# Kernel tuning notes

Measured on AMD Instinct MI355X. Metric: run time of the kernel, lower is better.

Reference implementation:

```python
import jax, jax.numpy as jnp
import numpy as np

# ---- static config (mirrors module init / config constants) ----
STATE_DIM = 512
D_H = 2048
INPUT_DIM = 1024
N_QUBITS = 6
N_VQC_LAYERS = 3
MSD = 128                 # mamba_state_dim (last dim of padded state)
PAD_SLICES = 16           # padded slice count in h_padded
MIN_T = 1e-6              # control_limits.min_value
REL_STEP = 0.1            # control_limits.hardware_relative_step
ABS_STEP = 1e-4           # control_limits.hardware_absolute_step
MAX_T = 0.05              # control_limits.max_value
DIM = 2 ** N_QUBITS

# qubit 0 = most significant bit (matches reshape-based gate application)
_BITS = ((np.arange(DIM)[:, None] >> np.arange(N_QUBITS)[None, ::-1]) & 1).astype(np.float32)
_sign = np.ones(DIM, np.float32)
for k in range(N_QUBITS):  # ring CZ entanglement
    k2 = (k + 1) % N_QUBITS
    _sign *= 1.0 - 2.0 * _BITS[:, k] * _BITS[:, k2]
CZ_SIGN = jnp.asarray(_sign)
Z_OBS = jnp.asarray((1.0 - 2.0 * _BITS).mean(axis=1))  # mean <Z_k> observable weights


def _apply_ry(state, ang, k):
    # state: [B, 2^n] real statevector; ang: [B] rotation angle on qubit k
    B = state.shape[0]
    s = state.reshape(B, 2 ** k, 2, 2 ** (N_QUBITS - k - 1))
    c = jnp.cos(ang / 2)[:, None, None]
    si = jnp.sin(ang / 2)[:, None, None]
    a0, a1 = s[:, :, 0, :], s[:, :, 1, :]
    out = jnp.stack([c * a0 - si * a1, si * a0 + c * a1], axis=2)
    return out.reshape(B, DIM)


def _vqc(feats, enc_W, enc_b, thetas):
    # EvolutionTimeVQCLayer: angle-encode features, layered RY + ring CZ, mean-Z expectation
    B = feats.shape[0]
    angles = feats @ enc_W + enc_b  # [B, n_qubits]
    state = jnp.zeros((B, DIM), feats.dtype).at[:, 0].set(1.0)
    for k in range(N_QUBITS):
        state = _apply_ry(state, angles[:, k], k)
    for l in range(N_VQC_LAYERS):
        for k in range(N_QUBITS):
            state = _apply_ry(state, jnp.broadcast_to(thetas[l, k], (B,)), k)
        state = state * CZ_SIGN[None, :]
    return (state * state) @ Z_OBS  # [B]


def _hamiltonian(q, p, x, W1, b1, W2, b2, W3, b3):
    z = jnp.concatenate([q, p, x], axis=-1)          # [B, 2*S + D]
    h1 = jnp.tanh(z @ W1 + b1)
    h2 = jnp.tanh(h1 @ W2 + b2)
    return (h2 @ W3)[:, 0] + b3                       # [B] scalar energy per sample


def setup_inputs() -> dict:
    key = jax.random.key(0)
    ks = jax.random.split(key, 12)
    def glorot(k, shape):
        std = np.sqrt(2.0 / (shape[0] + shape[-1]))
        return jax.random.normal(k, shape, jnp.float32) * std
    B = 2048
    h_in = 2 * STATE_DIM + INPUT_DIM
    gen_in = INPUT_DIM + 2 * STATE_DIM
    return {
        'x': jax.random.normal(ks[0], (B, INPUT_DIM), jnp.float32),
        'h_padded': jax.random.normal(ks[1], (B, PAD_SLICES, MSD), jnp.float32),
        'aux_padded': jnp.zeros((B, PAD_SLICES, MSD), jnp.float32),
        'W1': glorot(ks[2], (h_in, D_H)), 'b1': jnp.zeros((D_H,), jnp.float32),
        'W2': glorot(ks[3], (D_H, D_H)), 'b2': jnp.zeros((D_H,), jnp.float32),
        'W3': glorot(ks[4], (D_H, 1)), 'b3': jnp.zeros((), jnp.float32),
        'W_out': glorot(ks[5], (2 * STATE_DIM, INPUT_DIM)),
        'b_out': jnp.zeros((INPUT_DIM,), jnp.float32),
        'enc_W': glorot(ks[6], (gen_in, N_QUBITS)) * 0.1,
        'enc_b': jnp.zeros((N_QUBITS,), jnp.float32),
        'thetas': jax.random.normal(ks[7], (N_VQC_LAYERS, N_QUBITS), jnp.float32) * 0.1,
        'gain': jnp.asarray(0.1, jnp.float32),
        'shift': jnp.asarray(7.0, jnp.float32),
        'cap_param': jnp.asarray(0.02, jnp.float32),
        'time_bias': jnp.asarray(0.0005, jnp.float32),
        'last_stable': jnp.asarray(0.0005, jnp.float32),
    }


def reference(x, h_padded, aux_padded, W1, b1, W2, b2, W3, b3, W_out, b_out,
              enc_W, enc_b, thetas, gain, shift, cap_param, time_bias, last_stable):
    B = x.shape[0]
    total = 2 * STATE_DIM
    num_slices = total // MSD
    # unpack phase-space state from padded mamba-shaped state
    unpacked = h_padded[:, :num_slices, :].reshape(B, total)
    q_t, p_t = jnp.split(unpacked, 2, axis=-1)

    # ---- evolution-time generation via VQC ----
    ctrl = jnp.concatenate([x, q_t, p_t], axis=-1)
    samples = _vqc(ctrl, enc_W, enc_b, thetas)                       # [B]
    soft_gain = jax.nn.softplus(gain)
    soft_shift = jax.nn.softplus(shift)
    adjusted = jax.nn.softplus(soft_gain * samples - soft_shift)
    raw = jnp.mean(adjusted) + time_bias
    cap = jnp.maximum(jax.nn.softplus(cap_param), 1e-6)
    evo = cap * jax.nn.sigmoid(raw / cap)
    evo = jnp.where(jnp.isfinite(evo), evo, cap * jax.nn.sigmoid(time_bias / cap))
    prev = jnp.maximum(last_stable, MIN_T)
    cand = jnp.maximum(evo, MIN_T)
    max_step = jnp.maximum(prev * REL_STEP, ABS_STEP)
    cand = jnp.minimum(cand, prev + max_step)
    cand = jnp.minimum(cand, MAX_T)
    dt = jnp.where(jnp.isfinite(cand), cand, prev)                   # scalar

    # ---- fused HNN symplectic (leapfrog) step ----
    def H_sum(q, p):
        return _hamiltonian(q, p, x, W1, b1, W2, b2, W3, b3).sum()
    grad_qp = jax.grad(H_sum, argnums=(0, 1))
    dHdq0, _ = grad_qp(q_t, p_t)
    p_half = p_t - 0.5 * dt * dHdq0
    _, dHdp_h = grad_qp(q_t, p_half)
    q_next = q_t + dt * dHdp_h
    dHdq_n, _ = grad_qp(q_next, p_half)
    p_next = p_half - 0.5 * dt * dHdq_n

    out = jnp.concatenate([q_next, p_next], axis=-1) @ W_out + b_out  # [B, INPUT_DIM]

    # repack state into padded mamba layout
    new_slices = jnp.concatenate([q_next, p_next], axis=-1).reshape(B, num_slices, MSD)
    pad = jnp.zeros((B, PAD_SLICES - num_slices, MSD), out.dtype)
    h_next = jnp.concatenate([new_slices, pad], axis=1)
    return out, h_next
```

## Files before the change

kernel.cpp:

```cpp
#include <hip/hip_runtime.h>
#include <math.h>

#define NB 2048
#define ZD 2048
#define SD 512
#define NELEM_Z (NB * ZD)
#define MB_ (1024 * 1024)

typedef float f32x4 __attribute__((ext_vector_type(4)));
typedef __bf16 bf16x8 __attribute__((ext_vector_type(8)));
typedef __bf16 bf16x4 __attribute__((ext_vector_type(4)));

__device__ __forceinline__ float softplus_f(float x) {
  if (x > 20.f) return x;
  if (x < -20.f) return expf(x);
  return log1pf(expf(x));
}

__device__ __forceinline__ void gload_lds16(const __bf16* g, __bf16* l) {
  __builtin_amdgcn_global_load_lds(
      (__attribute__((address_space(1))) void*)(g),
      (__attribute__((address_space(3))) void*)(l), 16, 0, 0);
}

__device__ __forceinline__ int pack_fp8x4(float a, float b, float c, float d) {
  int p = __builtin_amdgcn_cvt_pk_fp8_f32(a, b, 0, false);
  p = __builtin_amdgcn_cvt_pk_fp8_f32(c, d, p, true);
  return p;
}
__device__ __forceinline__ float fp8_to_f32(unsigned char b) {
  return __builtin_amdgcn_cvt_f32_fp8((int)b, 0);
}

__global__ void build_z_kernel(const float* __restrict__ x,
                               const float* __restrict__ h_padded,
                               float* __restrict__ z,
                               __bf16* __restrict__ zb,
                               unsigned char* __restrict__ zf8,
                               float* __restrict__ acc) {
  int t = blockIdx.x * blockDim.x + threadIdx.x;
  if (t == 0) acc[0] = 0.f;
  int b = t >> 9;
  int i4 = t & 511;
  f32x4 v = (i4 < 256) ? ((const f32x4*)h_padded)[t]
                       : ((const f32x4*)x)[b * 256 + (i4 - 256)];
  ((f32x4*)z)[t] = v;
  bf16x4 o;
  o[0] = (__bf16)v[0]; o[1] = (__bf16)v[1];
  o[2] = (__bf16)v[2]; o[3] = (__bf16)v[3];
  ((bf16x4*)zb)[t] = o;
  ((int*)zf8)[t] = pack_fp8x4(v[0], v[1], v[2], v[3]);
}

__global__ void prep_w(const float* __restrict__ in,
                       __bf16* __restrict__ outT, int R, int C) {
  __shared__ float tile[32][33];
  int bx = blockIdx.x * 32, by = blockIdx.y * 32;
  int tx = threadIdx.x, ty = threadIdx.y;
  for (int r = ty; r < 32; r += 8)
    tile[r][tx] = in[(size_t)(by + r) * C + bx + tx];
  __syncthreads();
  for (int r = ty; r < 32; r += 8)
    outT[(size_t)(bx + r) * R + by + tx] = (__bf16)tile[tx][r];
}

__global__ void prep_w8(const float* __restrict__ in,
                        unsigned char* __restrict__ outN,
                        unsigned char* __restrict__ outT, int R, int C) {
  __shared__ float tile[32][33];
  int bx = blockIdx.x * 32, by = blockIdx.y * 32;
  int tx = threadIdx.x, ty = threadIdx.y;
  for (int r = ty; r < 32; r += 8) {
    float v = in[(size_t)(by + r) * C + bx + tx] * 16.f;
    tile[r][tx] = v;
    int p = __builtin_amdgcn_cvt_pk_fp8_f32(v, v, 0, false);
    outN[(size_t)(by + r) * C + bx + tx] = (unsigned char)(p & 0xff);
  }
  __syncthreads();
  for (int r = ty; r < 32; r += 8) {
    float v = tile[tx][r];
    int p = __builtin_amdgcn_cvt_pk_fp8_f32(v, v, 0, false);
    outT[(size_t)(bx + r) * R + by + tx] = (unsigned char)(p & 0xff);
  }
}

__global__ __launch_bounds__(256) void angles_kernel(
    const float* __restrict__ z,
    const float* __restrict__ enc_W,
    const float* __restrict__ enc_b,
    float* __restrict__ angles) {
  int w = threadIdx.x >> 6, lane = threadIdx.x & 63;
  int row = blockIdx.x * 4 + w;
  const float* zrow = z + (size_t)row * ZD;
  float pa[6] = {0.f, 0.f, 0.f, 0.f, 0.f, 0.f};
#pragma unroll
  for (int t = 0; t < 32; t++) {
    int j = t * 64 + lane;
    float c = (j < 1024) ? zrow[1024 + j] : zrow[j - 1024];
    const float* wp = enc_W + j * 6;
#pragma unroll
    for (int k = 0; k < 6; k++) pa[k] += c * wp[k];
  }
#pragma unroll
  for (int k = 0; k < 6; k++)
    for (int off = 32; off > 0; off >>= 1) pa[k] += __shfl_down(pa[k], off, 64);
  if (lane == 0) {
#pragma unroll
    for (int k = 0; k < 6; k++) angles[row * 6 + k] = pa[k] + enc_b[k];
  }
}

__global__ __launch_bounds__(64) void sim_kernel(
    const float* __restrict__ angles,
    const float* __restrict__ thetas,
    const float* __restrict__ gain,
    const float* __restrict__ shift,
    float* __restrict__ acc) {
  int row = blockIdx.x * 64 + threadIdx.x;
  const float* a = angles + row * 6;

  float s[64];
#pragma unroll
  for (int i = 0; i < 64; i++) s[i] = 0.f;
  s[0] = 1.f;

#pragma unroll
  for (int k = 0; k < 6; k++) {
    float half = 0.5f * a[k];
    float c = cosf(half), si = sinf(half);
    int m = 1 << (5 - k);
#pragma unroll
    for (int i = 0; i < 64; i++) {
      if ((i & m) == 0) {
        float a0 = s[i], a1 = s[i | m];
        s[i] = c * a0 - si * a1;
        s[i | m] = si * a0 + c * a1;
      }
    }
  }
#pragma unroll
  for (int l = 0; l < 3; l++) {
#pragma unroll
    for (int k = 0; k < 6; k++) {
      float half = 0.5f * thetas[l * 6 + k];
      float c = cosf(half), si = sinf(half);
      int m = 1 << (5 - k);
#pragma unroll
      for (int i = 0; i < 64; i++) {
        if ((i & m) == 0) {
          float a0 = s[i], a1 = s[i | m];
          s[i] = c * a0 - si * a1;
          s[i | m] = si * a0 + c * a1;
        }
      }
    }
#pragma unroll
    for (int i = 0; i < 64; i++) {
      int rot = ((i << 1) | (i >> 5)) & 63;
      if (__popc(i & rot) & 1) s[i] = -s[i];
    }
  }

  float val = 0.f;
#pragma unroll
  for (int i = 0; i < 64; i++) {
    float zo = (6.f - 2.f * (float)__popc(i)) * (1.f / 6.f);
    val += s[i] * s[i] * zo;
  }
  float sg = softplus_f(gain[0]);
  float ss = softplus_f(shift[0]);
  float adj = softplus_f(sg * val - ss);
  for (int off = 32; off > 0; off >>= 1) adj += __shfl_down(adj, off, 64);
  if (threadIdx.x == 0) atomicAdd(acc, adj);
}

__global__ void dt_kernel(const float* __restrict__ acc,
                          const float* __restrict__ cap_param,
                          const float* __restrict__ time_bias,
                          const float* __restrict__ last_stable,
                          float* __restrict__ dt_out) {
  float raw = acc[0] * (1.f / (float)NB) + time_bias[0];
  float cap = fmaxf(softplus_f(cap_param[0]), 1e-6f);
  float evo = cap / (1.f + expf(-raw / cap));
  if (!isfinite(evo)) evo = cap / (1.f + expf(-time_bias[0] / cap));
  float prev = fmaxf(last_stable[0], 1e-6f);
  float cand = fmaxf(evo, 1e-6f);
  float max_step = fmaxf(prev * 0.1f, 1e-4f);
  cand = fminf(cand, prev + max_step);
  cand = fminf(cand, 0.05f);
  dt_out[0] = isfinite(cand) ? cand : prev;
}

template <int EPI>
__global__ __launch_bounds__(256, 2) void mfma_gemm8(
    const unsigned char* __restrict__ A, int lda,
    const unsigned char* __restrict__ Bt, int ldb,
    void* __restrict__ Cv, int ldc,
    const float* __restrict__ bias,
    const float* __restrict__ w3,
    const unsigned char* __restrict__ aux, int ldaux,
    int Kslice) {
  __shared__ __align__(16) unsigned char sA[2 * 128 * 64];
  __shared__ __align__(16) unsigned char sB[2 * 64 * 64];

  const int tid = threadIdx.x;
  const int lane = tid & 63;
  const int w = tid >> 6;
  const int wm = w & 1, wn = w >> 1;
  const int row0 = blockIdx.y * 128;
  const int col0 = blockIdx.x * 64;
  const int koff = blockIdx.z * Kslice;

  const int mA0 = tid >> 2, cpA0 = tid & 3;
  const int mA1 = (256 + tid) >> 2, cpA1 = tid & 3;
  const int mB0 = tid >> 2, cpB0 = tid & 3;
  const unsigned char* gA0 = A + (size_t)(row0 + mA0) * lda + koff + cpA0 * 16;
  const unsigned char* gA1 = A + (size_t)(row0 + mA1) * lda + koff + cpA1 * 16;
  const unsigned char* gB0 = Bt + (size_t)(col0 + mB0) * ldb + koff + cpB0 * 16;
  const int wA0a = mA0 * 64 + (((2 * cpA0) + mA0) & 7) * 8;
  const int wA0b = mA0 * 64 + (((2 * cpA0 + 1) + mA0) & 7) * 8;
  const int wA1a = mA1 * 64 + (((2 * cpA1) + mA1) & 7) * 8;
  const int wA1b = mA1 * 64 + (((2 * cpA1 + 1) + mA1) & 7) * 8;
  const int wB0a = mB0 * 64 + (((2 * cpB0) + mB0) & 7) * 8;
  const int wB0b = mB0 * 64 + (((2 * cpB0 + 1) + mB0) & 7) * 8;

  const int q = lane >> 4, r = lane & 15;
  int aoff[4][2], boff[2][2];
#pragma unroll
  for (int i = 0; i < 4; i++) {
    int ma = wm * 64 + i * 16 + r;
#pragma unroll
    for (int h = 0; h < 2; h++)
      aoff[i][h] = ma * 64 + (((h * 4 + q) + ma) & 7) * 8;
  }
#pragma unroll
  for (int j = 0; j < 2; j++) {
    int mb = wn * 32 + j * 16 + r;
#pragma unroll
    for (int h = 0; h < 2; h++)
      boff[j][h] = mb * 64 + (((h * 4 + q) + mb) & 7) * 8;
  }

  f32x4 acc[4][2] = {};

  f32x4 rA0 = *(const f32x4*)gA0;
  f32x4 rA1 = *(const f32x4*)gA1;
  f32x4 rB0 = *(const f32x4*)gB0;
  *(long long*)(sA + wA0a) = ((const long long*)&rA0)[0];
  *(long long*)(sA + wA0b) = ((const long long*)&rA0)[1];
  *(long long*)(sA + wA1a) = ((const long long*)&rA1)[0];
  *(long long*)(sA + wA1b) = ((const long long*)&rA1)[1];
  *(long long*)(sB + wB0a) = ((const long long*)&rB0)[0];
  *(long long*)(sB + wB0b) = ((const long long*)&rB0)[1];
  __syncthreads();

  int cur = 0;
  for (int k0 = 0; k0 < Kslice; k0 += 64) {
    const bool more = (k0 + 64 < Kslice);
    if (more) {
      rA0 = *(const f32x4*)(gA0 + k0 + 64);
      rA1 = *(const f32x4*)(gA1 + k0 + 64);
      rB0 = *(const f32x4*)(gB0 + k0 + 64);
    }

    const unsigned char* bA = sA + cur * (128 * 64);
    const unsigned char* bB = sB + cur * (64 * 64);
#pragma unroll
    for (int h = 0; h < 2; h++) {
      long long af[4], bf[2];
#pragma unroll
      for (int i = 0; i < 4; i++) af[i] = *(const long long*)(bA + aoff[i][h]);
#pragma unroll
      for (int j = 0; j < 2; j++) bf[j] = *(const long long*)(bB + boff[j][h]);
#pragma unroll
      for (int i = 0; i < 4; i++)
#pragma unroll
        for (int j = 0; j < 2; j++)
          acc[i][j] = __builtin_amdgcn_mfma_f32_16x16x32_fp8_fp8(
              af[i], bf[j], acc[i][j], 0, 0, 0);
    }

    if (more) {
      unsigned char* nA = sA + (cur ^ 1) * (128 * 64);
      unsigned char* nB = sB + (cur ^ 1) * (64 * 64);
      *(long long*)(nA + wA0a) = ((const long long*)&rA0)[0];
      *(long long*)(nA + wA0b) = ((const long long*)&rA0)[1];
      *(long long*)(nA + wA1a) = ((const long long*)&rA1)[0];
      *(long long*)(nA + wA1b) = ((const long long*)&rA1)[1];
      *(long long*)(nB + wB0a) = ((const long long*)&rB0)[0];
      *(long long*)(nB + wB0b) = ((const long long*)&rB0)[1];
    }
    __syncthreads();
    cur ^= 1;
  }

  float* Cf = (float*)Cv;
  unsigned char* C8 = (unsigned char*)Cv;
  float* Pz = Cf + (size_t)blockIdx.z * (size_t)gridDim.y * 128 * ldc;

#pragma unroll
  for (int i = 0; i < 4; i++) {
    int rowb = row0 + wm * 64 + i * 16 + q * 4;
#pragma unroll
    for (int j = 0; j < 2; j++) {
      int col = col0 + wn * 32 + j * 16 + r;
      if (EPI == 0) {
#pragma unroll
        for (int g = 0; g < 4; g++)
          Pz[(size_t)(rowb + g) * ldc + col] = acc[i][j][g];
      } else {
        float o[4];
#pragma unroll
        for (int g = 0; g < 4; g++) {
          float v = acc[i][j][g] * 0.0625f;
          if (EPI == 1) {
            o[g] = tanhf(v + bias[col]);
          } else if (EPI == 2) {
            float t = tanhf(v + bias[col]);
            o[g] = 32.f * (1.f - t * t) * w3[col];
          } else {
            float h = fp8_to_f32(aux[(size_t)(rowb + g) * ldaux + col]);
            o[g] = v * (1.f - h * h);
          }
        }
        int p = pack_fp8x4(o[0], o[1], o[2], o[3]);
#pragma unroll
        for (int g = 0; g < 4; g++)
          C8[(size_t)(rowb + g) * ldc + col] =
              (unsigned char)((p >> (8 * g)) & 0xff);
      }
    }
  }
}

__global__ __launch_bounds__(256, 2) void mfma_gemm_bf16(
    const __bf16* __restrict__ A, int lda,
    const __bf16* __restrict__ Bt, int ldb,
    float* __restrict__ P, int ldc,
    int Kslice) {
  __shared__ __bf16 sA[2][128 * 64];
  __shared__ __bf16 sB[2][64 * 64];

  const int tid = threadIdx.x;
  const int lane = tid & 63;
  const int w = tid >> 6;
  const int wm = w & 1, wn = w >> 1;
  const int row0 = blockIdx.y * 128;
  const int col0 = blockIdx.x * 64;
  const int koff = blockIdx.z * Kslice;

  const __bf16* gA[4]; int lofA[4];
  const __bf16* gB[2]; int lofB[2];
#pragma unroll
  for (int i = 0; i < 4; i++) {
    int c = i * 256 + tid;
    int m = c >> 3, cc = c & 7;
    int o = cc ^ (m & 7);
    gA[i] = A + (size_t)(row0 + m) * lda + koff + o * 8;
    lofA[i] = c * 8;
  }
#pragma unroll
  for (int i = 0; i < 2; i++) {
    int c = i * 256 + tid;
    int m = c >> 3, cc = c & 7;
    int o = cc ^ (m & 7);
    gB[i] = Bt + (size_t)(col0 + m) * ldb + koff + o * 8;
    lofB[i] = c * 8;
  }

  const int q = lane >> 4, r = lane & 15;
  int aoff[4][2], boff[2][2];
#pragma unroll
  for (int i = 0; i < 4; i++) {
    int ma = wm * 64 + i * 16 + r;
#pragma unroll
    for (int h = 0; h < 2; h++)
      aoff[i][h] = (ma * 8 + ((h * 4 + q) ^ (ma & 7))) * 8;
  }
#pragma unroll
  for (int j = 0; j < 2; j++) {
    int mb = wn * 32 + j * 16 + r;
#pragma unroll
    for (int h = 0; h < 2; h++)
      boff[j][h] = (mb * 8 + ((h * 4 + q) ^ (mb & 7))) * 8;
  }

  f32x4 acc[4][2] = {};

#pragma unroll
  for (int i = 0; i < 4; i++) gload_lds16(gA[i], &sA[0][0] + lofA[i]);
#pragma unroll
  for (int i = 0; i < 2; i++) gload_lds16(gB[i], &sB[0][0] + lofB[i]);

  int cur = 0;
  for (int k0 = 0; k0 < Kslice; k0 += 64) {
    __syncthreads();
    if (k0 + 64 < Kslice) {
      int nxt = cur ^ 1;
#pragma unroll
      for (int i = 0; i < 4; i++)
        gload_lds16(gA[i] + k0 + 64, &sA[nxt][0] + lofA[i]);
#pragma unroll
      for (int i = 0; i < 2; i++)
        gload_lds16(gB[i] + k0 + 64, &sB[nxt][0] + lofB[i]);
    }
#pragma unroll
    for (int h = 0; h < 2; h++) {
      bf16x8 af[4], bfr[2];
#pragma unroll
      for (int i = 0; i < 4; i++)
        af[i] = *(const bf16x8*)(&sA[cur][0] + aoff[i][h]);
#pragma unroll
      for (int j = 0; j < 2; j++)
        bfr[j] = *(const bf16x8*)(&sB[cur][0] + boff[j][h]);
#pragma unroll
      for (int i = 0; i < 4; i++)
#pragma unroll
        for (int j = 0; j < 2; j++)
          acc[i][j] = __builtin_amdgcn_mfma_f32_16x16x32_bf16(af[i], bfr[j],
                                                              acc[i][j], 0, 0, 0);
    }
    cur ^= 1;
  }

  float* Pz = P + (size_t)blockIdx.z * (size_t)gridDim.y * 128 * ldc;
#pragma unroll
  for (int i = 0; i < 4; i++) {
    int rowb = row0 + wm * 64 + i * 16 + q * 4;
#pragma unroll
    for (int j = 0; j < 2; j++) {
      int col = col0 + wn * 32 + j * 16 + r;
#pragma unroll
      for (int g = 0; g < 4; g++)
        Pz[(size_t)(rowb + g) * ldc + col] = acc[i][j][g];
    }
  }
}

__global__ void update_kernel(float* __restrict__ z, __bf16* __restrict__ zb,
                              unsigned char* __restrict__ zf8,
                              const float* __restrict__ gp,
                              const float* __restrict__ dt,
                              float coef, int off) {
  int t = blockIdx.x * blockDim.x + threadIdx.x;
  int b = t >> 7;
  int j4 = t & 127;
  const f32x4* g4 = (const f32x4*)gp;
  constexpr int STRIDE = NB * SD / 4;
  f32x4 g = g4[t] + g4[t + STRIDE] + g4[t + 2 * STRIDE] + g4[t + 3 * STRIDE];
  int zi4 = (b * ZD + off) / 4 + j4;
  f32x4 v = ((f32x4*)z)[zi4];
  float s = coef * dt[0] * (1.f / 512.f);
  v[0] += s * g[0]; v[1] += s * g[1]; v[2] += s * g[2]; v[3] += s * g[3];
  ((f32x4*)z)[zi4] = v;
  bf16x4 o;
  o[0] = (__bf16)v[0]; o[1] = (__bf16)v[1];
  o[2] = (__bf16)v[2]; o[3] = (__bf16)v[3];
  ((bf16x4*)zb)[zi4] = o;
  ((int*)zf8)[zi4] = pack_fp8x4(v[0], v[1], v[2], v[3]);
}

__global__ void wout_reduce(const float* __restrict__ gp,
                            const float* __restrict__ b_out,
                            float* __restrict__ out) {
  int t = blockIdx.x * blockDim.x + threadIdx.x;
  constexpr int S = NB * 1024 / 4;
  const f32x4* g4 = (const f32x4*)gp;
  f32x4 v = g4[t] + g4[t + S];
  f32x4 bb = ((const f32x4*)b_out)[t & 255];
  v[0] += bb[0]; v[1] += bb[1]; v[2] += bb[2]; v[3] += bb[3];
  ((f32x4*)out)[t] = v;
}

__global__ void hnext_kernel(const float* __restrict__ z,
                             float* __restrict__ out) {
  int t = blockIdx.x * blockDim.x + threadIdx.x;
  int i4 = t & 511;
  f32x4 zero = {0.f, 0.f, 0.f, 0.f};
  ((f32x4*)out)[t] = (i4 < 256) ? ((const f32x4*)z)[t] : zero;
}

extern "C" void kernel_launch(void* const* d_in, const int* in_sizes, int n_in,
                              void* d_out, int out_size, void* d_ws,
                              size_t ws_size, hipStream_t stream) {
  const float* x        = (const float*)d_in[0];
  const float* h_padded = (const float*)d_in[1];
  const float* W1    = (const float*)d_in[3];
  const float* b1    = (const float*)d_in[4];
  const float* W2    = (const float*)d_in[5];
  const float* b2    = (const float*)d_in[6];
  const float* W3    = (const float*)d_in[7];
  const float* W_out = (const float*)d_in[9];
  const float* b_out = (const float*)d_in[10];
  const float* enc_W = (const float*)d_in[11];
  const float* enc_b = (const float*)d_in[12];
  const float* thetas = (const float*)d_in[13];
  const float* gain   = (const float*)d_in[14];
  const float* shift  = (const float*)d_in[15];
  const float* cap_p  = (const float*)d_in[16];
  const float* t_bias = (const float*)d_in[17];
  const float* l_stab = (const float*)d_in[18];

  float* out_mat  = (float*)d_out;
  float* out_hnxt = (float*)d_out + NB * 1024;

  char* base = (char*)d_ws;
  float* z      = (float*)(base);
  float* part   = (float*)(base + 16 * MB_);
  __bf16* zb    = (__bf16*)(base + 32 * MB_);
  __bf16* Wot   = (__bf16*)(base + 40 * MB_);
  float* angl   = (float*)(base + 42 * MB_);
  float* accp   = (float*)(base + 42 * MB_ + 65536);
  float* dtp    = accp + 1;
  unsigned char* zf8  = (unsigned char*)(base + 43 * MB_);
  unsigned char* h1_8 = zf8 + (size_t)NELEM_Z;
  unsigned char* g2_8 = h1_8 + (size_t)NELEM_Z;
  unsigned char* g1_8 = g2_8 + (size_t)NELEM_Z;
  unsigned char* W1n8 = g1_8 + (size_t)NELEM_Z;
  unsigned char* W1t8 = W1n8 + (size_t)NELEM_Z;
  unsigned char* W2n8 = W1t8 + (size_t)NELEM_Z;
  unsigned char* W2t8 = W2n8 + (size_t)NELEM_Z;

  dim3 thr256(256);
  dim3 thrT(32, 8);

  prep_w8<<<dim3(64, 64), thrT, 0, stream>>>(W1, W1n8, W1t8, ZD, ZD);
  prep_w8<<<dim3(64, 64), thrT, 0, stream>>>(W2, W2n8, W2t8, ZD, ZD);
  prep_w<<<dim3(32, 32), thrT, 0, stream>>>(W_out, Wot, 1024, 1024);

  build_z_kernel<<<dim3(NELEM_Z / 4 / 256), thr256, 0, stream>>>(
      x, h_padded, z, zb, zf8, accp);
  angles_kernel<<<dim3(NB / 4), thr256, 0, stream>>>(z, enc_W, enc_b, angl);
  sim_kernel<<<dim3(NB / 64), dim3(64), 0, stream>>>(angl, thetas, gain, shift,
                                                     accp);
  dt_kernel<<<dim3(1), dim3(1), 0, stream>>>(accp, cap_p, t_bias, l_stab, dtp);

  const int   j0r[3]  = {0, 512, 0};
  const int   offs[3] = {512, 0, 512};
  const float coef[3] = {-0.5f, 1.0f, -0.5f};

  dim3 gridSq(32, 16, 1);
  dim3 gridGr(8, 16, 4);

  for (int i = 0; i < 3; i++) {
    mfma_gemm8<1><<<gridSq, thr256, 0, stream>>>(
        zf8, ZD, W1t8, ZD, h1_8, ZD, b1, nullptr, nullptr, 0, ZD);
    mfma_gemm8<2><<<gridSq, thr256, 0, stream>>>(
        h1_8, ZD, W2t8, ZD, g2_8, ZD, b2, W3, nullptr, 0, ZD);
    mfma_gemm8<3><<<gridSq, thr256, 0, stream>>>(
        g2_8, ZD, W2n8, ZD, g1_8, ZD, nullptr, nullptr, h1_8, ZD, ZD);
    mfma_gemm8<0><<<gridGr, thr256, 0, stream>>>(
        g1_8, ZD, W1n8 + (size_t)j0r[i] * ZD, ZD, part, SD, nullptr, nullptr,
        nullptr, 0, 512);
    update_kernel<<<dim3(NB * SD / 4 / 256), thr256, 0, stream>>>(
        z, zb, zf8, part, dtp, coef[i], offs[i]);
  }

  mfma_gemm_bf16<<<dim3(16, 16, 2), thr256, 0, stream>>>(zb, ZD, Wot, 1024,
                                                         part, 1024, 512);
  wout_reduce<<<dim3(NB * 1024 / 4 / 256), thr256, 0, stream>>>(part, b_out,
                                                                out_mat);

  hnext_kernel<<<dim3(NELEM_Z / 4 / 256), thr256, 0, stream>>>(z, out_hnxt);
}
```

Baseline: 481.4 us.

## Double GEMM K-tile to 128 with padded LDS and fuse angle encoding into z build

The FP8 MFMA GEMM now stages 128-wide K tiles in LDS with a 144-byte padded row stride instead of 64-wide XOR-swizzled tiles. Each fragment is fetched with one 16-byte LDS read that feeds two MFMAs, which halves the loop iterations and barriers. Separately, the VQC angle projection is folded into the z-building kernel, removing one launch and a reread of z. In exchange, LDS use per block roughly doubles and more prefetch registers are live, which may lower occupancy under the 2-blocks bound.

After: 445.9 us. -7.4%, faster.

```diff
diff --git a/kernel.cpp b/kernel.cpp
--- a/kernel.cpp
+++ b/kernel.cpp
@@ -10,6 +10,7 @@
 typedef float f32x4 __attribute__((ext_vector_type(4)));
 typedef __bf16 bf16x8 __attribute__((ext_vector_type(8)));
 typedef __bf16 bf16x4 __attribute__((ext_vector_type(4)));
+typedef long long i64;
 
 __device__ __forceinline__ float softplus_f(float x) {
   if (x > 20.f) return x;
@@ -32,24 +33,55 @@
   return __builtin_amdgcn_cvt_f32_fp8((int)b, 0);
 }
 
-__global__ void build_z_kernel(const float* __restrict__ x,
-                               const float* __restrict__ h_padded,
-                               float* __restrict__ z,
-                               __bf16* __restrict__ zb,
-                               unsigned char* __restrict__ zf8,
-                               float* __restrict__ acc) {
-  int t = blockIdx.x * blockDim.x + threadIdx.x;
-  if (t == 0) acc[0] = 0.f;
-  int b = t >> 9;
-  int i4 = t & 511;
-  f32x4 v = (i4 < 256) ? ((const f32x4*)h_padded)[t]
-                       : ((const f32x4*)x)[b * 256 + (i4 - 256)];
-  ((f32x4*)z)[t] = v;
-  bf16x4 o;
-  o[0] = (__bf16)v[0]; o[1] = (__bf16)v[1];
-  o[2] = (__bf16)v[2]; o[3] = (__bf16)v[3];
-  ((bf16x4*)zb)[t] = o;
-  ((int*)zf8)[t] = pack_fp8x4(v[0], v[1], v[2], v[3]);
+__global__ __launch_bounds__(256) void build_z_kernel(
+    const float* __restrict__ x,
+    const float* __restrict__ h_padded,
+    const float* __restrict__ enc_W,
+    const float* __restrict__ enc_b,
+    float* __restrict__ z,
+    __bf16* __restrict__ zb,
+    unsigned char* __restrict__ zf8,
+    float* __restrict__ angles,
+    float* __restrict__ acc) {
+  int b = blockIdx.x;
+  int tid = threadIdx.x;
+  if (b == 0 && tid == 0) acc[0] = 0.f;
+  int lane = tid & 63, w = tid >> 6;
+  __shared__ float red[4][6];
+
+  float pa[6] = {0.f, 0.f, 0.f, 0.f, 0.f, 0.f};
+#pragma unroll
+  for (int cc = 0; cc < 2; cc++) {
+    int c = cc * 256 + tid;
+    int i = c * 4;
+    f32x4 v = (i < 1024) ? ((const f32x4*)(h_padded + (size_t)b * 2048))[c]
+                         : ((const f32x4*)(x + (size_t)b * 1024))[c - 256];
+    size_t zi = (size_t)b * 512 + c;
+    ((f32x4*)z)[zi] = v;
+    bf16x4 o;
+    o[0] = (__bf16)v[0]; o[1] = (__bf16)v[1];
+    o[2] = (__bf16)v[2]; o[3] = (__bf16)v[3];
+    ((bf16x4*)zb)[zi] = o;
+    ((int*)zf8)[zi] = pack_fp8x4(v[0], v[1], v[2], v[3]);
+    int cj = (i < 1024) ? (1024 + i) : (i - 1024);
+#pragma unroll
+    for (int e = 0; e < 4; e++) {
+      const float* wp = enc_W + (size_t)(cj + e) * 6;
+#pragma unroll
+      for (int k = 0; k < 6; k++) pa[k] += v[e] * wp[k];
+    }
+  }
+#pragma unroll
+  for (int k = 0; k < 6; k++)
+    for (int off = 32; off > 0; off >>= 1) pa[k] += __shfl_down(pa[k], off, 64);
+  if (lane == 0) {
+#pragma unroll
+    for (int k = 0; k < 6; k++) red[w][k] = pa[k];
+  }
+  __syncthreads();
+  if (tid < 6)
+    angles[b * 6 + tid] =
+        red[0][tid] + red[1][tid] + red[2][tid] + red[3][tid] + enc_b[tid];
 }
 
 __global__ void prep_w(const float* __restrict__ in,
@@ -81,32 +113,6 @@
     float v = tile[tx][r];
     int p = __builtin_amdgcn_cvt_pk_fp8_f32(v, v, 0, false);
     outT[(size_t)(bx + r) * R + by + tx] = (unsigned char)(p & 0xff);
-  }
-}
-
-__global__ __launch_bounds__(256) void angles_kernel(
-    const float* __restrict__ z,
-    const float* __restrict__ enc_W,
-    const float* __restrict__ enc_b,
-    float* __restrict__ angles) {
-  int w = threadIdx.x >> 6, lane = threadIdx.x & 63;
-  int row = blockIdx.x * 4 + w;
-  const float* zrow = z + (size_t)row * ZD;
-  float pa[6] = {0.f, 0.f, 0.f, 0.f, 0.f, 0.f};
-#pragma unroll
-  for (int t = 0; t < 32; t++) {
-    int j = t * 64 + lane;
-    float c = (j < 1024) ? zrow[1024 + j] : zrow[j - 1024];
-    const float* wp = enc_W + j * 6;
-#pragma unroll
-    for (int k = 0; k < 6; k++) pa[k] += c * wp[k];
-  }
-#pragma unroll
-  for (int k = 0; k < 6; k++)
-    for (int off = 32; off > 0; off >>= 1) pa[k] += __shfl_down(pa[k], off, 64);
-  if (lane == 0) {
-#pragma unroll
-    for (int k = 0; k < 6; k++) angles[row * 6 + k] = pa[k] + enc_b[k];
   }
 }
 
@@ -200,8 +206,8 @@
     const float* __restrict__ w3,
     const unsigned char* __restrict__ aux, int ldaux,
     int Kslice) {
-  __shared__ __align__(16) unsigned char sA[2 * 128 * 64];
-  __shared__ __align__(16) unsigned char sB[2 * 64 * 64];
+  __shared__ __align__(16) unsigned char sA[2][128 * 144];
+  __shared__ __align__(16) unsigned char sB[2][64 * 144];
 
   const int tid = threadIdx.x;
   const int lane = tid & 63;
@@ -211,18 +217,28 @@
   const int col0 = blockIdx.x * 64;
   const int koff = blockIdx.z * Kslice;
 
-  const int mA0 = tid >> 2, cpA0 = tid & 3;
-  const int mA1 = (256 + tid) >> 2, cpA1 = tid & 3;
-  const int mB0 = tid >> 2, cpB0 = tid & 3;
-  const unsigned char* gA0 = A + (size_t)(row0 + mA0) * lda + koff + cpA0 * 16;
-  const unsigned char* gA1 = A + (size_t)(row0 + mA1) * lda + koff + cpA1 * 16;
-  const unsigned char* gB0 = Bt + (size_t)(col0 + mB0) * ldb + koff + cpB0 * 16;
-  const int wA0a = mA0 * 64 + (((2 * cpA0) + mA0) & 7) * 8;
-  const int wA0b = mA0 * 64 + (((2 * cpA0 + 1) + mA0) & 7) * 8;
-  const int wA1a = mA1 * 64 + (((2 * cpA1) + mA1) & 7) * 8;
-  const int wA1b = mA1 * 64 + (((2 * cpA1 + 1) + mA1) & 7) * 8;
-  const int wB0a = mB0 * 64 + (((2 * cpB0) + mB0) & 7) * 8;
-  const int wB0b = mB0 * 64 + (((2 * cpB0 + 1) + mB0) & 7) * 8;
+  const unsigned char* gA[4]; int wA0[4], wA1[4];
+  const unsigned char* gB[2]; int wB0[2], wB1[2];
+#pragma unroll
+  for (int i = 0; i < 4; i++) {
+    int c = i * 256 + tid;
+    int m = c >> 3, cp = c & 7;
+    gA[i] = A + (size_t)(row0 + m) * lda + koff + cp * 16;
+    int h = cp >> 1;
+    int Hofs = (h >> 1) * 16 + (h & 1) * 8;
+    wA0[i] = m * 144 + ((2 * cp) & 3) * 32 + Hofs;
+    wA1[i] = m * 144 + ((2 * cp + 1) & 3) * 32 + Hofs;
+  }
+#pragma unroll
+  for (int i = 0; i < 2; i++) {
+    int c = i * 256 + tid;
+    int m = c >> 3, cp = c & 7;
+    gB[i] = Bt + (size_t)(col0 + m) * ldb + koff + cp * 16;
+    int h = cp >> 1;
+    int Hofs = (h >> 1) * 16 + (h & 1) * 8;
+    wB0[i] = m * 144 + ((2 * cp) & 3) * 32 + Hofs;
+    wB1[i] = m * 144 + ((2 * cp + 1) & 3) * 32 + Hofs;
+  }
 
   const int q = lane >> 4, r = lane & 15;
   int aoff[4][2], boff[2][2];
@@ -230,65 +246,88 @@
   for (int i = 0; i < 4; i++) {
     int ma = wm * 64 + i * 16 + r;
 #pragma unroll
-    for (int h = 0; h < 2; h++)
-      aoff[i][h] = ma * 64 + (((h * 4 + q) + ma) & 7) * 8;
+    for (int H = 0; H < 2; H++) aoff[i][H] = ma * 144 + q * 32 + H * 16;
   }
 #pragma unroll
   for (int j = 0; j < 2; j++) {
     int mb = wn * 32 + j * 16 + r;
 #pragma unroll
-    for (int h = 0; h < 2; h++)
-      boff[j][h] = mb * 64 + (((h * 4 + q) + mb) & 7) * 8;
+    for (int H = 0; H < 2; H++) boff[j][H] = mb * 144 + q * 32 + H * 16;
   }
 
   f32x4 acc[4][2] = {};
-
-  f32x4 rA0 = *(const f32x4*)gA0;
-  f32x4 rA1 = *(const f32x4*)gA1;
-  f32x4 rB0 = *(const f32x4*)gB0;
-  *(long long*)(sA + wA0a) = ((const long long*)&rA0)[0];
-  *(long long*)(sA + wA0b) = ((const long long*)&rA0)[1];
-  *(long long*)(sA + wA1a) = ((const long long*)&rA1)[0];
-  *(long long*)(sA + wA1b) = ((const long long*)&rA1)[1];
-  *(long long*)(sB + wB0a) = ((const long long*)&rB0)[0];
-  *(long long*)(sB + wB0b) = ((const long long*)&rB0)[1];
+  f32x4 rA[4], rB[2];
+
+#pragma unroll
+  for (int i = 0; i < 4; i++) rA[i] = *(const f32x4*)gA[i];
+#pragma unroll
+  for (int i = 0; i < 2; i++) rB[i] = *(const f32x4*)gB[i];
+#pragma unroll
+  for (int i = 0; i < 4; i++) {
+    *(i64*)(&sA[0][0] + wA0[i]) = ((const i64*)&rA[i])[0];
+    *(i64*)(&sA[0][0] + wA1[i]) = ((const i64*)&rA[i])[1];
+  }
+#pragma unroll
+  for (int i = 0; i < 2; i++) {
+    *(i64*)(&sB[0][0] + wB0[i]) = ((const i64*)&rB[i])[0];
+    *(i64*)(&sB[0][0] + wB1[i]) = ((const i64*)&rB[i])[1];
+  }
   __syncthreads();
 
   int cur = 0;
-  for (int k0 = 0; k0 < Kslice; k0 += 64) {
-    const bool more = (k0 + 64 < Kslice);
+  for (int k0 = 0; k0 < Kslice; k0 += 128) {
+    const bool more = (k0 + 128 < Kslice);
     if (more) {
-      rA0 = *(const f32x4*)(gA0 + k0 + 64);
-      rA1 = *(const f32x4*)(gA1 + k0 + 64);
-      rB0 = *(const f32x4*)(gB0 + k0 + 64);
-    }
-
-    const unsigned char* bA = sA + cur * (128 * 64);
-    const unsigned char* bB = sB + cur * (64 * 64);
-#pragma unroll
-    for (int h = 0; h < 2; h++) {
-      long long af[4], bf[2];
-#pragma unroll
-      for (int i = 0; i < 4; i++) af[i] = *(const long long*)(bA + aoff[i][h]);
-#pragma unroll
-      for (int j = 0; j < 2; j++) bf[j] = *(const long long*)(bB + boff[j][h]);
+#pragma unroll
+      for (int i = 0; i < 4; i++) rA[i] = *(const f32x4*)(gA[i] + k0 + 128);
+#pragma unroll
+      for (int i = 0; i < 2; i++) rB[i] = *(const f32x4*)(gB[i] + k0 + 128);
+    }
+
+    const unsigned char* bA = &sA[cur][0];
+    const unsigned char* bB = &sB[cur][0];
+#pragma unroll
+    for (int H = 0; H < 2; H++) {
+      i64 a0[4], a1[4], b0[2], b1[2];
+#pragma unroll
+      for (int i = 0; i < 4; i++) {
+        f32x4 v = *(const f32x4*)(bA + aoff[i][H]);
+        a0[i] = ((const i64*)&v)[0];
+        a1[i] = ((const i64*)&v)[1];
+      }
+#pragma unroll
+      for (int j = 0; j < 2; j++) {
+        f32x4 v = *(const f32x4*)(bB + boff[j][H]);
+        b0[j] = ((const i64*)&v)[0];
+        b1[j] = ((const i64*)&v)[1];
+      }
 #pragma unroll
       for (int i = 0; i < 4; i++)
 #pragma unroll
         for (int j = 0; j < 2; j++)
           acc[i][j] = __builtin_amdgcn_mfma_f32_16x16x32_fp8_fp8(
-              af[i], bf[j], acc[i][j], 0, 0, 0);
+              a0[i], b0[j], acc[i][j], 0, 0, 0);
+#pragma unroll
+      for (int i = 0; i < 4; i++)
+#pragma unroll
+        for (int j = 0; j < 2; j++)
+          acc[i][j] = __builtin_amdgcn_mfma_f32_16x16x32_fp8_fp8(
+              a1[i], b1[j], acc[i][j], 0, 0, 0);
     }
 
     if (more) {
-      unsigned char* nA = sA + (cur ^ 1) * (128 * 64);
-      unsigned char* nB = sB + (cur ^ 1) * (64 * 64);
-      *(long long*)(nA + wA0a) = ((const long long*)&rA0)[0];
-      *(long long*)(nA + wA0b) = ((const long long*)&rA0)[1];
-      *(long long*)(nA + wA1a) = ((const long long*)&rA1)[0];
-      *(long long*)(nA + wA1b) = ((const long long*)&rA1)[1];
-      *(long long*)(nB + wB0a) = ((const long long*)&rB0)[0];
-      *(long long*)(nB + wB0b) = ((const long long*)&rB0)[1];
+      unsigned char* nA = &sA[cur ^ 1][0];
+      unsigned char* nB = &sB[cur ^ 1][0];
+#pragma unroll
+      for (int i = 0; i < 4; i++) {
+        *(i64*)(nA + wA0[i]) = ((const i64*)&rA[i])[0];
+        *(i64*)(nA + wA1[i]) = ((const i64*)&rA[i])[1];
+      }
+#pragma unroll
+      for (int i = 0; i < 2; i++) {
+        *(i64*)(nB + wB0[i]) = ((const i64*)&rB[i])[0];
+        *(i64*)(nB + wB1[i]) = ((const i64*)&rB[i])[1];
+      }
     }
     __syncthreads();
     cur ^= 1;
@@ -528,9 +567,8 @@
   prep_w8<<<dim3(64, 64), thrT, 0, stream>>>(W2, W2n8, W2t8, ZD, ZD);
   prep_w<<<dim3(32, 32), thrT, 0, stream>>>(W_out, Wot, 1024, 1024);
 
-  build_z_kernel<<<dim3(NELEM_Z / 4 / 256), thr256, 0, stream>>>(
-      x, h_padded, z, zb, zf8, accp);
-  angles_kernel<<<dim3(NB / 4), thr256, 0, stream>>>(z, enc_W, enc_b, angl);
+  build_z_kernel<<<dim3(NB), thr256, 0, stream>>>(x, h_padded, enc_W, enc_b, z,
+                                                  zb, zf8, angl, accp);
   sim_kernel<<<dim3(NB / 64), dim3(64), 0, stream>>>(angl, thetas, gain, shift,
                                                      accp);
   dt_kernel<<<dim3(1), dim3(1), 0, stream>>>(accp, cap_p, t_bias, l_stab, dtp);
```
